# Performance work log

Measured on AMD Instinct MI355X. Metric: run time of the kernel, lower is better.

The kernel has to match this reference:

```python
import jax, jax.numpy as jnp
import numpy as np

# Config (from Mamba3Config defaults)
D_MODEL = 768
EXPAND = 4
D_INNER = EXPAND * D_MODEL          # 3072
D_HEAD = 64
N_HEADS = D_INNER // D_HEAD         # 48
N_EXPERTS = 8
TOP_K = 2
R3 = 256                            # latent MoE input dim
R2 = 1024                           # latent MoE output dim
EPS = 1e-5
TANH_SCALE = 10.0                   # fast_scaled_tanh default
ROUTER_TEMP = 0.5                   # get_router_temperature(step=None) -> t_end


def _rms_norm(x, w):
    return x * jax.lax.rsqrt(jnp.mean(x * x, axis=-1, keepdims=True) + EPS) * w


def _scaled_tanh(x):
    return TANH_SCALE * jnp.tanh(x * (1.0 / TANH_SCALE))


def setup_inputs() -> dict:
    key = jax.random.key(0)
    ks = jax.random.split(key, 13)
    s = 0.02
    B, L = 2, 4096
    return {
        "x": jax.random.normal(ks[0], (B, L, D_MODEL), dtype=jnp.float32),
        "rms1_w": jnp.ones((D_MODEL,), jnp.float32),
        "W_in": s * jax.random.normal(ks[1], (D_MODEL, 2 * D_INNER + N_HEADS), jnp.float32),
        "dt_bias": jax.random.uniform(ks[2], (N_HEADS,), jnp.float32, -4.0, -1.0),  # dt in [dt_min, dt_max]-ish
        "W_out": s * jax.random.normal(ks[3], (D_INNER, D_MODEL), jnp.float32),
        "ls1": 0.01 * jnp.ones((D_MODEL,), jnp.float32),
        "rms2_w": jnp.ones((D_MODEL,), jnp.float32),
        "W_down": s * jax.random.normal(ks[4], (D_MODEL, R3), jnp.float32),
        "W_router": s * jax.random.normal(ks[5], (D_MODEL, N_EXPERTS), jnp.float32),
        "G": s * jax.random.normal(ks[6], (N_EXPERTS, R3, R2), jnp.float32),
        "W_up": s * jax.random.normal(ks[7], (R2, D_MODEL), jnp.float32),
        "ls2": 0.01 * jnp.ones((D_MODEL,), jnp.float32),
    }


def reference(x, rms1_w, W_in, dt_bias, W_out, ls1, rms2_w, W_down, W_router, G, W_up, ls2):
    B, L, _ = x.shape
    # ---- Mamba selective-scan branch ----
    xn = _rms_norm(x, rms1_w)
    proj = xn @ W_in                                   # [B,L,2*Di+H]
    u, z, dt = jnp.split(proj, [D_INNER, 2 * D_INNER], axis=-1)
    log_alpha = -jax.nn.softplus(dt + dt_bias)         # [B,L,H], per-head scalar decay
    alpha = jnp.exp(log_alpha)[..., None]              # [B,L,H,1]
    u4 = u.reshape(B, L, N_HEADS, D_HEAD)

    def combine(left, right):                          # first_order_combine_op
        a_l, b_l = left
        a_r, b_r = right
        return (a_r * a_l, a_r * b_l + b_r)

    _, h = jax.lax.associative_scan(
        combine, (jnp.broadcast_to(alpha, u4.shape), u4), axis=1)
    y = h.reshape(B, L, D_INNER) * jax.nn.silu(z)
    y = _scaled_tanh(y)
    x1 = x + ls1 * (y @ W_out)

    # ---- Fused latent MoE (Tucker) branch ----
    x2n = _rms_norm(x1, rms2_w)
    lat = _scaled_tanh(x2n @ W_down)                   # [B,L,r3]
    logits = (x2n @ W_router) * (1.0 / ROUTER_TEMP)    # [B,L,E]
    vals, idx = jax.lax.top_k(logits, TOP_K)
    probs = jax.nn.softmax(vals, axis=-1)              # [B,L,K]
    # dense combine weights: w[b,l,e] = sum_k probs_k * [idx_k == e]
    w = jnp.sum(jax.nn.one_hot(idx, N_EXPERTS, dtype=lat.dtype) * probs[..., None], axis=-2)
    # out[b,l,c] = sum_e w[b,l,e] * (lat[b,l,:] @ G[e])  (== fused gather grouped-GEMM)
    moe = jnp.einsum('blr,erc,ble->blc', lat, G, w)    # [B,L,r2]
    out = x1 + ls2 * (moe @ W_up)
    return out
```

## Files before the change

### kernel.cpp

```cpp
#include <hip/hip_runtime.h>
#include <stdint.h>

typedef unsigned short ushort_t;
typedef __attribute__((ext_vector_type(8))) __bf16 bf16x8;
typedef __attribute__((ext_vector_type(4))) float floatx4;
typedef __attribute__((ext_vector_type(4))) unsigned short ushort4v;
typedef __attribute__((ext_vector_type(8))) unsigned short ushort8v;

#define TT 8192L
#define LB 4096L
#define DD 768L
#define DI 3072L
#define NH 48L
#define R3C 256L
#define R2C 1024L
#define NP 6272L
#define CHS 64L

__device__ __forceinline__ float b2f(ushort_t u) {
  union { unsigned u32; float f; } v; v.u32 = ((unsigned)u) << 16; return v.f;
}
__device__ __forceinline__ ushort_t f2b(float f) {
  union { float f; unsigned u32; } v; v.f = f;
  unsigned r = v.u32 + 0x7FFFu + ((v.u32 >> 16) & 1u);
  return (ushort_t)(r >> 16);
}
__device__ __forceinline__ float fast_tanh(float x) {
  float e = __expf(2.0f * x);
  return 1.0f - 2.0f / (e + 1.0f);
}
__device__ __forceinline__ void g2l16(const void* g, void* l) {
  __builtin_amdgcn_global_load_lds(
      (const __attribute__((address_space(1))) unsigned int*)g,
      (__attribute__((address_space(3))) unsigned int*)l, 16, 0, 0);
}

__global__ __launch_bounds__(256) void k_tr(const float* __restrict__ src,
                                            ushort_t* __restrict__ dst,
                                            int K, int N) {
  __shared__ float tile[64][65];
  int k0 = blockIdx.x * 64, n0 = blockIdx.y * 64;
  int c = threadIdx.x & 63, r4 = threadIdx.x >> 6;
#pragma unroll
  for (int s = 0; s < 16; s++) {
    int r = s * 4 + r4;
    int n = n0 + c;
    tile[c][r] = (n < N) ? src[(long)(k0 + r) * N + n] : 0.0f;
  }
  __syncthreads();
#pragma unroll
  for (int s = 0; s < 16; s++) {
    int r = s * 4 + r4;
    dst[(long)(n0 + r) * K + k0 + c] = f2b(tile[r][c]);
  }
}

__global__ __launch_bounds__(256) void k_rms(const float* __restrict__ x,
                                             const float* __restrict__ w,
                                             ushort_t* __restrict__ out) {
  int t = blockIdx.x, tid = threadIdx.x;
  int lane = tid & 63, wid = tid >> 6;
  const float* xr = x + (long)t * DD;
  float v0 = xr[tid], v1 = xr[tid + 256], v2 = xr[tid + 512];
  float ss = v0 * v0 + v1 * v1 + v2 * v2;
  for (int o = 32; o; o >>= 1) ss += __shfl_down(ss, o);
  __shared__ float red[4];
  if (lane == 0) red[wid] = ss;
  __syncthreads();
  float tot = red[0] + red[1] + red[2] + red[3];
  float rr = rsqrtf(tot / 768.0f + 1e-5f);
  ushort_t* orow = out + (long)t * DD;
  orow[tid]       = f2b(v0 * rr * w[tid]);
  orow[tid + 256] = f2b(v1 * rr * w[tid + 256]);
  orow[tid + 512] = f2b(v2 * rr * w[tid + 512]);
}

__global__ __launch_bounds__(256) void k_rms2_router(const ushort_t* __restrict__ x1,
                                                     const float* __restrict__ w,
                                                     const float* __restrict__ wr,
                                                     ushort_t* __restrict__ x2n,
                                                     float* __restrict__ wrt) {
  int t = blockIdx.x, tid = threadIdx.x;
  int lane = tid & 63, wid = tid >> 6;
  const ushort_t* xr = x1 + (long)t * DD;
  float v[3];
  int dd[3] = {tid, tid + 256, tid + 512};
  v[0] = b2f(xr[dd[0]]); v[1] = b2f(xr[dd[1]]); v[2] = b2f(xr[dd[2]]);
  float ss = v[0] * v[0] + v[1] * v[1] + v[2] * v[2];
  for (int o = 32; o; o >>= 1) ss += __shfl_down(ss, o);
  __shared__ float red[4];
  __shared__ float wred[4][8];
  __shared__ float slog[8];
  if (lane == 0) red[wid] = ss;
  __syncthreads();
  float tot = red[0] + red[1] + red[2] + red[3];
  float rr = rsqrtf(tot / 768.0f + 1e-5f);
  float p[8] = {0, 0, 0, 0, 0, 0, 0, 0};
  ushort_t* orow = x2n + (long)t * DD;
#pragma unroll
  for (int i = 0; i < 3; i++) {
    float xnv = v[i] * rr * w[dd[i]];
    orow[dd[i]] = f2b(xnv);
    const float* wrow = wr + (long)dd[i] * 8;
#pragma unroll
    for (int e = 0; e < 8; e++) p[e] += xnv * wrow[e];
  }
#pragma unroll
  for (int e = 0; e < 8; e++) {
    float s = p[e];
    for (int o = 32; o; o >>= 1) s += __shfl_down(s, o);
    if (lane == 0) wred[wid][e] = s;
  }
  __syncthreads();
  if (tid < 8)
    slog[tid] = (wred[0][tid] + wred[1][tid] + wred[2][tid] + wred[3][tid]) * 2.0f;
  __syncthreads();
  if (tid == 0) {
    float l[8];
#pragma unroll
    for (int e = 0; e < 8; e++) l[e] = slog[e];
    int e0 = 0; float b0 = l[0];
#pragma unroll
    for (int e = 1; e < 8; e++) if (l[e] > b0) { b0 = l[e]; e0 = e; }
    int e1 = -1; float b1 = -1e30f;
#pragma unroll
    for (int e = 0; e < 8; e++) if (e != e0 && l[e] > b1) { b1 = l[e]; e1 = e; }
    float ex = __expf(b1 - b0);
    float pd = 1.0f / (1.0f + ex);
    float* wo = wrt + (long)t * 8;
#pragma unroll
    for (int e = 0; e < 8; e++) wo[e] = 0.0f;
    wo[e0] = pd;
    wo[e1] = ex * pd;
  }
}

__global__ __launch_bounds__(256) void k_alpha(const ushort_t* __restrict__ proj,
                                               const float* __restrict__ dtb,
                                               float* __restrict__ alpha) {
  int gid = blockIdx.x * 256 + threadIdx.x;
  int tg = gid / 48;
  int h = gid - tg * 48;
  float dt = b2f(proj[(long)tg * NP + 2 * DI + h]) + dtb[h];
  float sp = (dt > 20.0f) ? dt : log1pf(__expf(dt));
  alpha[(long)h * LB + tg] = __expf(-sp);
}

__device__ __forceinline__ void stage_tile(const ushort_t* __restrict__ g, long rowstride,
                                           ushort_t* __restrict__ lds, int lane) {
  const int lrow = lane >> 3;
  const int dcol = (lane & 7) * 8;
#pragma unroll
  for (int c8 = 0; c8 < 8; c8++) {
    ushort8v v = *(const ushort8v*)(g + (long)(c8 * 8 + lrow) * rowstride + dcol);
    *(ushort8v*)&lds[(c8 * 64 + lane) * 8] = v;
  }
}

__global__ __launch_bounds__(64) void k_scan1(const ushort_t* __restrict__ proj,
                                              const float* __restrict__ alpha,
                                              float* __restrict__ ssum,
                                              float* __restrict__ asum) {
  __shared__ __align__(16) ushort_t u_lds[64 * 64];
  __shared__ float s_alpha[64];
  const int lane = threadIdx.x;
  const int idx = blockIdx.x;
  const int c = idx & 63;
  const int h = idx >> 6;
  s_alpha[lane] = alpha[(long)h * LB + (long)c * CHS + lane];
  const ushort_t* ug = proj + (long)c * CHS * NP + (long)h * 64;
  stage_tile(ug, NP, u_lds, lane);
  __syncthreads();
  float s = 0.0f, A = 1.0f;
#pragma unroll
  for (int tt = 0; tt < 64; tt++) {
    float a = s_alpha[tt];
    float u = b2f(u_lds[tt * 64 + lane]);
    s = fmaf(a, s, u);
    A *= a;
  }
  ssum[(long)idx * 64 + lane] = s;
  if (lane == 0) asum[idx] = A;
}

__global__ __launch_bounds__(64) void k_scan2(const float* __restrict__ ssum,
                                              const float* __restrict__ asum,
                                              float* __restrict__ carry) {
  int h = blockIdx.x, lane = threadIdx.x;
  float cv = 0.0f;
  for (int c = 0; c < 64; c++) {
    carry[((long)h * 64 + c) * 64 + lane] = cv;
    float A = asum[h * 64 + c];
    float s = ssum[((long)h * 64 + c) * 64 + lane];
    cv = A * cv + s;
  }
}

__global__ __launch_bounds__(64) void k_scan3(const ushort_t* __restrict__ proj,
                                              const float* __restrict__ alpha,
                                              const float* __restrict__ carry,
                                              ushort_t* __restrict__ y) {
  __shared__ __align__(16) ushort_t u_lds[64 * 64];
  __shared__ __align__(16) ushort_t z_lds[64 * 64];
  __shared__ float s_alpha[64];
  const int lane = threadIdx.x;
  const int idx = blockIdx.x;
  const int c = idx & 63;
  const int h = idx >> 6;
  s_alpha[lane] = alpha[(long)h * LB + (long)c * CHS + lane];
  const ushort_t* ug = proj + (long)c * CHS * NP + (long)h * 64;
  const ushort_t* zg = ug + DI;
  ushort_t* yg = y + (long)c * CHS * DI + (long)h * 64;
  stage_tile(ug, NP, u_lds, lane);
  stage_tile(zg, NP, z_lds, lane);
  __syncthreads();
  float hs = carry[(long)idx * 64 + lane];
#pragma unroll
  for (int tt = 0; tt < 64; tt++) {
    float a = s_alpha[tt];
    float u = b2f(u_lds[tt * 64 + lane]);
    hs = fmaf(a, hs, u);
    float zv = b2f(z_lds[tt * 64 + lane]);
    float sig = 1.0f / (1.0f + __expf(-zv));
    float yv = hs * zv * sig;
    yv = 10.0f * fast_tanh(yv * 0.1f);
    yg[(long)tt * DI + lane] = f2b(yv);
  }
}

__global__ __launch_bounds__(256) void k_abig(const ushort_t* __restrict__ lat,
                                              const float* __restrict__ wrt,
                                              ushort_t* __restrict__ abig) {
  long gid = (long)blockIdx.x * 256 + threadIdx.x;
  long idx = gid * 4;
  int t = (int)(idx >> 11);
  int off = (int)(idx & 2047);
  int e = off >> 8, r = off & 255;
  float wv = wrt[(long)t * 8 + e];
  ushort4v lv = *(const ushort4v*)(lat + (long)t * R3C + r);
  ushort4v ov;
  ov.x = f2b(wv * b2f(lv.x));
  ov.y = f2b(wv * b2f(lv.y));
  ov.z = f2b(wv * b2f(lv.z));
  ov.w = f2b(wv * b2f(lv.w));
  *(ushort4v*)(abig + (long)t * 2048 + off) = ov;
}

template <int MODE>
__global__ __launch_bounds__(256, 4) void k_gemm(const ushort_t* __restrict__ A,
                                                 const ushort_t* __restrict__ Bt,
                                                 void* __restrict__ Cout, int K, int kstride,
                                                 int ldc, long zoff) {
  __shared__ __align__(16) ushort_t sA[128 * 32];
  __shared__ __align__(16) ushort_t sB[128 * 32];
  const int tid = threadIdx.x;
  const int lane = tid & 63, wid = tid >> 6;
  const int lm = lane & 15, q = lane >> 4;
  const int wm = wid >> 1, wn = wid & 1;
  const long row0 = (long)blockIdx.x * 128;
  const long col0 = (long)blockIdx.y * 128;
  const int z = blockIdx.z;
  A += (long)z * K;
  Bt += (long)z * K;

  floatx4 acc[4][4] = {};

  const int srow = wid * 32 + (lane >> 2);
  const int skoff = (lane & 3) * 8;
  const ushort_t* Ag0 = A + (row0 + srow) * (long)kstride + skoff;
  const ushort_t* Ag1 = Ag0 + 16L * kstride;
  const ushort_t* Bg0 = Bt + (col0 + srow) * (long)kstride + skoff;
  const ushort_t* Bg1 = Bg0 + 16L * kstride;
  ushort_t* sA0 = sA + wid * 1024;
  ushort_t* sB0 = sB + wid * 1024;

  for (int k0 = 0; k0 < K; k0 += 32) {
    g2l16(Ag0 + k0, sA0);
    g2l16(Ag1 + k0, sA0 + 512);
    g2l16(Bg0 + k0, sB0);
    g2l16(Bg1 + k0, sB0 + 512);
    __syncthreads();
    bf16x8 af[4], bfr[4];
#pragma unroll
    for (int i = 0; i < 4; i++)
      af[i] = *(const bf16x8*)(const void*)&sA[(wm * 64 + i * 16 + lm) * 32 + q * 8];
#pragma unroll
    for (int j = 0; j < 4; j++)
      bfr[j] = *(const bf16x8*)(const void*)&sB[(wn * 64 + j * 16 + lm) * 32 + q * 8];
#pragma unroll
    for (int i = 0; i < 4; i++)
#pragma unroll
      for (int j = 0; j < 4; j++)
        acc[i][j] = __builtin_amdgcn_mfma_f32_16x16x32_bf16(af[i], bfr[j], acc[i][j], 0, 0, 0);
    __syncthreads();
  }
#pragma unroll
  for (int i = 0; i < 4; i++) {
#pragma unroll
    for (int r = 0; r < 4; r++) {
      long row = row0 + wm * 64 + i * 16 + q * 4 + r;
#pragma unroll
      for (int j = 0; j < 4; j++) {
        long col = col0 + wn * 64 + j * 16 + lm;
        float v = acc[i][j][r];
        if (MODE == 0) {
          ((ushort_t*)Cout)[row * (long)ldc + col] = f2b(v);
        } else {
          ((float*)Cout)[(long)z * zoff + row * (long)ldc + col] = v;
        }
      }
    }
  }
}

__global__ __launch_bounds__(256) void k_comb_res(const float* __restrict__ P, long zoff, int nz,
                                                  const float* __restrict__ x,
                                                  const float* __restrict__ ls,
                                                  ushort_t* __restrict__ x1) {
  long i = ((long)blockIdx.x * 256 + threadIdx.x) * 4;
  float s[4] = {0, 0, 0, 0};
  for (int zz = 0; zz < nz; zz++) {
    const float* p = P + (long)zz * zoff + i;
#pragma unroll
    for (int j = 0; j < 4; j++) s[j] += p[j];
  }
  int c = (int)(i % DD);
#pragma unroll
  for (int j = 0; j < 4; j++) x1[i + j] = f2b(x[i + j] + ls[c + j] * s[j]);
}

__global__ __launch_bounds__(256) void k_comb_tanh(const float* __restrict__ P, long zoff, int nz,
                                                   ushort_t* __restrict__ lat) {
  long i = ((long)blockIdx.x * 256 + threadIdx.x) * 4;
  float s[4] = {0, 0, 0, 0};
  for (int zz = 0; zz < nz; zz++) {
    const float* p = P + (long)zz * zoff + i;
#pragma unroll
    for (int j = 0; j < 4; j++) s[j] += p[j];
  }
#pragma unroll
  for (int j = 0; j < 4; j++) lat[i + j] = f2b(10.0f * fast_tanh(0.1f * s[j]));
}

__global__ __launch_bounds__(256) void k_comb_out(const float* __restrict__ P, long zoff, int nz,
                                                  const ushort_t* __restrict__ x1,
                                                  const float* __restrict__ ls,
                                                  float* __restrict__ outp) {
  long i = ((long)blockIdx.x * 256 + threadIdx.x) * 4;
  float s[4] = {0, 0, 0, 0};
  for (int zz = 0; zz < nz; zz++) {
    const float* p = P + (long)zz * zoff + i;
#pragma unroll
    for (int j = 0; j < 4; j++) s[j] += p[j];
  }
  int c = (int)(i % DD);
#pragma unroll
  for (int j = 0; j < 4; j++) outp[i + j] = b2f(x1[i + j]) + ls[c + j] * s[j];
}

#define OFF_WINT   0L
#define OFF_WOUTT  9633792L
#define OFF_WDNT   14352384L
#define OFF_WUPT   14745600L
#define OFF_GT     16318464L
#define OFF_X1     20512768L
#define OFF_WRT    33095680L
#define OFF_ALPHA  33357824L
#define OFF_SSUM   34144256L
#define OFF_ASUM   34930688L
#define OFF_CARRY  34942976L
#define OFF_XN     35729408L
#define OFF_Y      48312320L
#define OFF_PROJ   73478144L
#define OFF_ABIG   OFF_PROJ
#define OFF_LAT    (OFF_PROJ + 33554432L)
#define OFF_PART   OFF_PROJ
#define OFF_X2N    OFF_XN
#define OFF_MOE    OFF_Y
#define WS_NEEDED  124858368L

extern "C" void kernel_launch(void* const* d_in, const int* in_sizes, int n_in,
                              void* d_out, int out_size, void* d_ws, size_t ws_size,
                              hipStream_t stream) {
  const float* x     = (const float*)d_in[0];
  const float* rms1w = (const float*)d_in[1];
  const float* W_in  = (const float*)d_in[2];
  const float* dtb   = (const float*)d_in[3];
  const float* W_out = (const float*)d_in[4];
  const float* ls1   = (const float*)d_in[5];
  const float* rms2w = (const float*)d_in[6];
  const float* W_dn  = (const float*)d_in[7];
  const float* W_rtr = (const float*)d_in[8];
  const float* G     = (const float*)d_in[9];
  const float* W_up  = (const float*)d_in[10];
  const float* ls2   = (const float*)d_in[11];
  if (ws_size < (size_t)WS_NEEDED) return;

  char* ws = (char*)d_ws;
  ushort_t* W_inT  = (ushort_t*)(ws + OFF_WINT);
  ushort_t* W_outT = (ushort_t*)(ws + OFF_WOUTT);
  ushort_t* W_dnT  = (ushort_t*)(ws + OFF_WDNT);
  ushort_t* W_upT  = (ushort_t*)(ws + OFF_WUPT);
  ushort_t* GT     = (ushort_t*)(ws + OFF_GT);
  ushort_t* x1     = (ushort_t*)(ws + OFF_X1);
  float*    wrt    = (float*)(ws + OFF_WRT);
  float*    alpha  = (float*)(ws + OFF_ALPHA);
  float*    ssum   = (float*)(ws + OFF_SSUM);
  float*    asum   = (float*)(ws + OFF_ASUM);
  float*    carry  = (float*)(ws + OFF_CARRY);
  ushort_t* xn     = (ushort_t*)(ws + OFF_XN);
  ushort_t* y      = (ushort_t*)(ws + OFF_Y);
  ushort_t* proj   = (ushort_t*)(ws + OFF_PROJ);
  ushort_t* abig   = (ushort_t*)(ws + OFF_ABIG);
  ushort_t* lat    = (ushort_t*)(ws + OFF_LAT);
  float*    part   = (float*)(ws + OFF_PART);
  ushort_t* x2n    = (ushort_t*)(ws + OFF_X2N);
  ushort_t* moe    = (ushort_t*)(ws + OFF_MOE);
  float*    outp   = (float*)d_out;

  k_tr<<<dim3(12, 98), 256, 0, stream>>>(W_in, W_inT, 768, 6192);
  k_tr<<<dim3(48, 12), 256, 0, stream>>>(W_out, W_outT, 3072, 768);
  k_tr<<<dim3(12, 4), 256, 0, stream>>>(W_dn, W_dnT, 768, 256);
  k_tr<<<dim3(16, 12), 256, 0, stream>>>(W_up, W_upT, 1024, 768);
  k_tr<<<dim3(32, 16), 256, 0, stream>>>(G, GT, 2048, 1024);

  k_rms<<<8192, 256, 0, stream>>>(x, rms1w, xn);

  for (int b = 0; b < 2; b++) {
    const ushort_t* xnb = xn + (long)b * LB * DD;
    k_gemm<0><<<dim3(32, 49, 1), 256, 0, stream>>>(xnb, W_inT, proj, 768, 768, (int)NP, 0);
    k_alpha<<<768, 256, 0, stream>>>(proj, dtb, alpha);
    k_scan1<<<3072, 64, 0, stream>>>(proj, alpha, ssum, asum);
    k_scan2<<<48, 64, 0, stream>>>(ssum, asum, carry);
    k_scan3<<<3072, 64, 0, stream>>>(proj, alpha, carry, y);
    k_gemm<4><<<dim3(32, 6, 4), 256, 0, stream>>>(y, W_outT, part, 768, 3072, 768, LB * DD);
    k_comb_res<<<3072, 256, 0, stream>>>(part, LB * DD, 4, x + (long)b * LB * DD, ls1,
                                         x1 + (long)b * LB * DD);
  }

  k_rms2_router<<<8192, 256, 0, stream>>>(x1, rms2w, W_rtr, x2n, wrt);
  k_gemm<4><<<dim3(64, 2, 3), 256, 0, stream>>>(x2n, W_dnT, part, 256, 768, 256, TT * R3C);
  k_comb_tanh<<<2048, 256, 0, stream>>>(part, TT * R3C, 3, lat);
  k_abig<<<16384, 256, 0, stream>>>(lat, wrt, abig);
  k_gemm<0><<<dim3(64, 8, 1), 256, 0, stream>>>(abig, GT, moe, 2048, 2048, 1024, 0);
  k_gemm<4><<<dim3(64, 6, 2), 256, 0, stream>>>(moe, W_upT, part, 512, 1024, 768, TT * DD);
  k_comb_out<<<6144, 256, 0, stream>>>(part, TT * DD, 2, x1, ls2, outp);
}
```

Before: 575.8 us.

## Fuse transposes, inline alpha, merge residual with rms2/router, widen GEMM K-step

Folds the five weight-transpose launches into one kernel and computes alpha inline inside both scan kernels, so the alpha buffer and its kernel go away. The split-K residual combine is fused with RMSNorm2 and the router, which drops one pass that wrote and re-read x1. The GEMM now stages 64 K-elements per barrier in two sub-tiles, halving barriers but doubling LDS use, which may lower occupancy. Alpha is now computed twice per chunk, once in each scan kernel.

```diff
diff --git a/kernel.cpp b/kernel.cpp
--- a/kernel.cpp
+++ b/kernel.cpp
@@ -35,11 +35,20 @@
       (__attribute__((address_space(3))) unsigned int*)l, 16, 0, 0);
 }
 
-__global__ __launch_bounds__(256) void k_tr(const float* __restrict__ src,
-                                            ushort_t* __restrict__ dst,
-                                            int K, int N) {
+__global__ __launch_bounds__(256) void k_tr_all(const float* __restrict__ s0, ushort_t* __restrict__ d0,
+                                                const float* __restrict__ s1, ushort_t* __restrict__ d1,
+                                                const float* __restrict__ s2, ushort_t* __restrict__ d2,
+                                                const float* __restrict__ s3, ushort_t* __restrict__ d3,
+                                                const float* __restrict__ s4, ushort_t* __restrict__ d4) {
   __shared__ float tile[64][65];
-  int k0 = blockIdx.x * 64, n0 = blockIdx.y * 64;
+  int id = blockIdx.x;
+  const float* src; ushort_t* dst; int K, N, gx;
+  if (id < 1176)      {            src = s0; dst = d0; K = 768;  N = 6192; gx = 12; }
+  else if (id < 1752) { id -= 1176; src = s1; dst = d1; K = 3072; N = 768;  gx = 48; }
+  else if (id < 1800) { id -= 1752; src = s2; dst = d2; K = 768;  N = 256;  gx = 12; }
+  else if (id < 1992) { id -= 1800; src = s3; dst = d3; K = 1024; N = 768;  gx = 16; }
+  else                { id -= 1992; src = s4; dst = d4; K = 2048; N = 1024; gx = 32; }
+  int k0 = (id % gx) * 64, n0 = (id / gx) * 64;
   int c = threadIdx.x & 63, r4 = threadIdx.x >> 6;
 #pragma unroll
   for (int s = 0; s < 16; s++) {
@@ -75,17 +84,26 @@
   orow[tid + 512] = f2b(v2 * rr * w[tid + 512]);
 }
 
-__global__ __launch_bounds__(256) void k_rms2_router(const ushort_t* __restrict__ x1,
-                                                     const float* __restrict__ w,
-                                                     const float* __restrict__ wr,
-                                                     ushort_t* __restrict__ x2n,
-                                                     float* __restrict__ wrt) {
+__global__ __launch_bounds__(256) void k_fuse2(const float* __restrict__ P,
+                                               const float* __restrict__ x,
+                                               const float* __restrict__ ls1,
+                                               const float* __restrict__ w2,
+                                               const float* __restrict__ wr,
+                                               ushort_t* __restrict__ x1,
+                                               ushort_t* __restrict__ x2n,
+                                               float* __restrict__ wrt) {
   int t = blockIdx.x, tid = threadIdx.x;
   int lane = tid & 63, wid = tid >> 6;
-  const ushort_t* xr = x1 + (long)t * DD;
+  int dd[3] = {tid, tid + 256, tid + 512};
   float v[3];
-  int dd[3] = {tid, tid + 256, tid + 512};
-  v[0] = b2f(xr[dd[0]]); v[1] = b2f(xr[dd[1]]); v[2] = b2f(xr[dd[2]]);
+#pragma unroll
+  for (int i = 0; i < 3; i++) {
+    long ix = (long)t * DD + dd[i];
+    float s = P[ix] + P[LB * DD + ix] + P[2 * LB * DD + ix] + P[3 * LB * DD + ix];
+    float xv = x[ix] + ls1[dd[i]] * s;
+    x1[ix] = f2b(xv);
+    v[i] = xv;
+  }
   float ss = v[0] * v[0] + v[1] * v[1] + v[2] * v[2];
   for (int o = 32; o; o >>= 1) ss += __shfl_down(ss, o);
   __shared__ float red[4];
@@ -99,7 +117,7 @@
   ushort_t* orow = x2n + (long)t * DD;
 #pragma unroll
   for (int i = 0; i < 3; i++) {
-    float xnv = v[i] * rr * w[dd[i]];
+    float xnv = v[i] * rr * w2[dd[i]];
     orow[dd[i]] = f2b(xnv);
     const float* wrow = wr + (long)dd[i] * 8;
 #pragma unroll
@@ -135,17 +153,6 @@
   }
 }
 
-__global__ __launch_bounds__(256) void k_alpha(const ushort_t* __restrict__ proj,
-                                               const float* __restrict__ dtb,
-                                               float* __restrict__ alpha) {
-  int gid = blockIdx.x * 256 + threadIdx.x;
-  int tg = gid / 48;
-  int h = gid - tg * 48;
-  float dt = b2f(proj[(long)tg * NP + 2 * DI + h]) + dtb[h];
-  float sp = (dt > 20.0f) ? dt : log1pf(__expf(dt));
-  alpha[(long)h * LB + tg] = __expf(-sp);
-}
-
 __device__ __forceinline__ void stage_tile(const ushort_t* __restrict__ g, long rowstride,
                                            ushort_t* __restrict__ lds, int lane) {
   const int lrow = lane >> 3;
@@ -157,8 +164,15 @@
   }
 }
 
+__device__ __forceinline__ float alpha_of(const ushort_t* __restrict__ proj, int tok, int h,
+                                          const float* __restrict__ dtb) {
+  float dt = b2f(proj[(long)tok * NP + 2 * DI + h]) + dtb[h];
+  float sp = (dt > 20.0f) ? dt : log1pf(__expf(dt));
+  return __expf(-sp);
+}
+
 __global__ __launch_bounds__(64) void k_scan1(const ushort_t* __restrict__ proj,
-                                              const float* __restrict__ alpha,
+                                              const float* __restrict__ dtb,
                                               float* __restrict__ ssum,
                                               float* __restrict__ asum) {
   __shared__ __align__(16) ushort_t u_lds[64 * 64];
@@ -167,7 +181,7 @@
   const int idx = blockIdx.x;
   const int c = idx & 63;
   const int h = idx >> 6;
-  s_alpha[lane] = alpha[(long)h * LB + (long)c * CHS + lane];
+  s_alpha[lane] = alpha_of(proj, (int)(c * CHS) + lane, h, dtb);
   const ushort_t* ug = proj + (long)c * CHS * NP + (long)h * 64;
   stage_tile(ug, NP, u_lds, lane);
   __syncthreads();
@@ -197,7 +211,7 @@
 }
 
 __global__ __launch_bounds__(64) void k_scan3(const ushort_t* __restrict__ proj,
-                                              const float* __restrict__ alpha,
+                                              const float* __restrict__ dtb,
                                               const float* __restrict__ carry,
                                               ushort_t* __restrict__ y) {
   __shared__ __align__(16) ushort_t u_lds[64 * 64];
@@ -207,7 +221,7 @@
   const int idx = blockIdx.x;
   const int c = idx & 63;
   const int h = idx >> 6;
-  s_alpha[lane] = alpha[(long)h * LB + (long)c * CHS + lane];
+  s_alpha[lane] = alpha_of(proj, (int)(c * CHS) + lane, h, dtb);
   const ushort_t* ug = proj + (long)c * CHS * NP + (long)h * 64;
   const ushort_t* zg = ug + DI;
   ushort_t* yg = y + (long)c * CHS * DI + (long)h * 64;
@@ -251,8 +265,8 @@
                                                  const ushort_t* __restrict__ Bt,
                                                  void* __restrict__ Cout, int K, int kstride,
                                                  int ldc, long zoff) {
-  __shared__ __align__(16) ushort_t sA[128 * 32];
-  __shared__ __align__(16) ushort_t sB[128 * 32];
+  __shared__ __align__(16) ushort_t sA[2 * 128 * 32];
+  __shared__ __align__(16) ushort_t sB[2 * 128 * 32];
   const int tid = threadIdx.x;
   const int lane = tid & 63, wid = tid >> 6;
   const int lm = lane & 15, q = lane >> 4;
@@ -265,33 +279,36 @@
 
   floatx4 acc[4][4] = {};
 
-  const int srow = wid * 32 + (lane >> 2);
-  const int skoff = (lane & 3) * 8;
-  const ushort_t* Ag0 = A + (row0 + srow) * (long)kstride + skoff;
-  const ushort_t* Ag1 = Ag0 + 16L * kstride;
-  const ushort_t* Bg0 = Bt + (col0 + srow) * (long)kstride + skoff;
-  const ushort_t* Bg1 = Bg0 + 16L * kstride;
-  ushort_t* sA0 = sA + wid * 1024;
-  ushort_t* sB0 = sB + wid * 1024;
-
-  for (int k0 = 0; k0 < K; k0 += 32) {
-    g2l16(Ag0 + k0, sA0);
-    g2l16(Ag1 + k0, sA0 + 512);
-    g2l16(Bg0 + k0, sB0);
-    g2l16(Bg1 + k0, sB0 + 512);
+  const int trow = tid >> 2;
+  const int tcol = (tid & 3) * 8;
+  const ushort_t* Ag = A + (row0 + trow) * (long)kstride + tcol;
+  const ushort_t* Bg = Bt + (col0 + trow) * (long)kstride + tcol;
+  const long rstep = 64L * kstride;
+
+  for (int k0 = 0; k0 < K; k0 += 64) {
+#pragma unroll
+    for (int kk = 0; kk < 2; kk++)
+#pragma unroll
+      for (int rh = 0; rh < 2; rh++) {
+        g2l16(Ag + rh * rstep + k0 + kk * 32, sA + kk * 4096 + rh * 2048 + wid * 512);
+        g2l16(Bg + rh * rstep + k0 + kk * 32, sB + kk * 4096 + rh * 2048 + wid * 512);
+      }
     __syncthreads();
-    bf16x8 af[4], bfr[4];
-#pragma unroll
-    for (int i = 0; i < 4; i++)
-      af[i] = *(const bf16x8*)(const void*)&sA[(wm * 64 + i * 16 + lm) * 32 + q * 8];
-#pragma unroll
-    for (int j = 0; j < 4; j++)
-      bfr[j] = *(const bf16x8*)(const void*)&sB[(wn * 64 + j * 16 + lm) * 32 + q * 8];
-#pragma unroll
-    for (int i = 0; i < 4; i++)
+#pragma unroll
+    for (int kk = 0; kk < 2; kk++) {
+      bf16x8 af[4], bfr[4];
+#pragma unroll
+      for (int i = 0; i < 4; i++)
+        af[i] = *(const bf16x8*)(const void*)&sA[kk * 4096 + (wm * 64 + i * 16 + lm) * 32 + q * 8];
 #pragma unroll
       for (int j = 0; j < 4; j++)
-        acc[i][j] = __builtin_amdgcn_mfma_f32_16x16x32_bf16(af[i], bfr[j], acc[i][j], 0, 0, 0);
+        bfr[j] = *(const bf16x8*)(const void*)&sB[kk * 4096 + (wn * 64 + j * 16 + lm) * 32 + q * 8];
+#pragma unroll
+      for (int i = 0; i < 4; i++)
+#pragma unroll
+        for (int j = 0; j < 4; j++)
+          acc[i][j] = __builtin_amdgcn_mfma_f32_16x16x32_bf16(af[i], bfr[j], acc[i][j], 0, 0, 0);
+    }
     __syncthreads();
   }
 #pragma unroll
@@ -313,22 +330,6 @@
   }
 }
 
-__global__ __launch_bounds__(256) void k_comb_res(const float* __restrict__ P, long zoff, int nz,
-                                                  const float* __restrict__ x,
-                                                  const float* __restrict__ ls,
-                                                  ushort_t* __restrict__ x1) {
-  long i = ((long)blockIdx.x * 256 + threadIdx.x) * 4;
-  float s[4] = {0, 0, 0, 0};
-  for (int zz = 0; zz < nz; zz++) {
-    const float* p = P + (long)zz * zoff + i;
-#pragma unroll
-    for (int j = 0; j < 4; j++) s[j] += p[j];
-  }
-  int c = (int)(i % DD);
-#pragma unroll
-  for (int j = 0; j < 4; j++) x1[i + j] = f2b(x[i + j] + ls[c + j] * s[j]);
-}
-
 __global__ __launch_bounds__(256) void k_comb_tanh(const float* __restrict__ P, long zoff, int nz,
                                                    ushort_t* __restrict__ lat) {
   long i = ((long)blockIdx.x * 256 + threadIdx.x) * 4;
@@ -365,7 +366,6 @@
 #define OFF_GT     16318464L
 #define OFF_X1     20512768L
 #define OFF_WRT    33095680L
-#define OFF_ALPHA  33357824L
 #define OFF_SSUM   34144256L
 #define OFF_ASUM   34930688L
 #define OFF_CARRY  34942976L
@@ -404,7 +404,6 @@
   ushort_t* GT     = (ushort_t*)(ws + OFF_GT);
   ushort_t* x1     = (ushort_t*)(ws + OFF_X1);
   float*    wrt    = (float*)(ws + OFF_WRT);
-  float*    alpha  = (float*)(ws + OFF_ALPHA);
   float*    ssum   = (float*)(ws + OFF_SSUM);
   float*    asum   = (float*)(ws + OFF_ASUM);
   float*    carry  = (float*)(ws + OFF_CARRY);
@@ -418,27 +417,22 @@
   ushort_t* moe    = (ushort_t*)(ws + OFF_MOE);
   float*    outp   = (float*)d_out;
 
-  k_tr<<<dim3(12, 98), 256, 0, stream>>>(W_in, W_inT, 768, 6192);
-  k_tr<<<dim3(48, 12), 256, 0, stream>>>(W_out, W_outT, 3072, 768);
-  k_tr<<<dim3(12, 4), 256, 0, stream>>>(W_dn, W_dnT, 768, 256);
-  k_tr<<<dim3(16, 12), 256, 0, stream>>>(W_up, W_upT, 1024, 768);
-  k_tr<<<dim3(32, 16), 256, 0, stream>>>(G, GT, 2048, 1024);
-
+  k_tr_all<<<2504, 256, 0, stream>>>(W_in, W_inT, W_out, W_outT, W_dn, W_dnT,
+                                     W_up, W_upT, G, GT);
   k_rms<<<8192, 256, 0, stream>>>(x, rms1w, xn);
 
   for (int b = 0; b < 2; b++) {
     const ushort_t* xnb = xn + (long)b * LB * DD;
     k_gemm<0><<<dim3(32, 49, 1), 256, 0, stream>>>(xnb, W_inT, proj, 768, 768, (int)NP, 0);
-    k_alpha<<<768, 256, 0, stream>>>(proj, dtb, alpha);
-    k_scan1<<<3072, 64, 0, stream>>>(proj, alpha, ssum, asum);
+    k_scan1<<<3072, 64, 0, stream>>>(proj, dtb, ssum, asum);
     k_scan2<<<48, 64, 0, stream>>>(ssum, asum, carry);
-    k_scan3<<<3072, 64, 0, stream>>>(proj, alpha, carry, y);
+    k_scan3<<<3072, 64, 0, stream>>>(proj, dtb, carry, y);
     k_gemm<4><<<dim3(32, 6, 4), 256, 0, stream>>>(y, W_outT, part, 768, 3072, 768, LB * DD);
-    k_comb_res<<<3072, 256, 0, stream>>>(part, LB * DD, 4, x + (long)b * LB * DD, ls1,
-                                         x1 + (long)b * LB * DD);
-  }
-
-  k_rms2_router<<<8192, 256, 0, stream>>>(x1, rms2w, W_rtr, x2n, wrt);
+    k_fuse2<<<4096, 256, 0, stream>>>(part, x + (long)b * LB * DD, ls1, rms2w, W_rtr,
+                                      x1 + (long)b * LB * DD, x2n + (long)b * LB * DD,
+                                      wrt + (long)b * LB * 8);
+  }
+
   k_gemm<4><<<dim3(64, 2, 3), 256, 0, stream>>>(x2n, W_dnT, part, 256, 768, 256, TT * R3C);
   k_comb_tanh<<<2048, 256, 0, stream>>>(part, TT * R3C, 3, lat);
   k_abig<<<16384, 256, 0, stream>>>(lat, wrt, abig);
```

Measured after the change: 519.0 us. -9.9%, faster.
